# Kernel optimization log

Measured on AMD Instinct MI355X. Metric: run time of the kernel, lower is better.

Reference implementation:

```python
import jax, jax.numpy as jnp
import numpy as np

N_ACTIVE = 200000   # active voxels
GRID = 96           # spatial grid extent per axis
C = 128             # inplanes == outplanes
EPS = 1e-4          # scn BatchNormalization default eps


def _build_rulebook(n, g, seed=0):
    """Submanifold 3x3x3 rulebook: for each of 27 offsets, pairs (in_site, out_site)
    where coord[in] = coord[out] + offset and both sites are active. Padded to
    length n with dummy index n."""
    rng = np.random.default_rng(seed)
    lin = rng.choice(g ** 3, size=n, replace=False)
    coords = np.stack(np.unravel_index(lin, (g, g, g)), axis=1)  # [n,3]
    lut = -np.ones(g ** 3, dtype=np.int64)
    lut[lin] = np.arange(n)
    in_rows, out_rows = [], []
    for dx in (-1, 0, 1):
        for dy in (-1, 0, 1):
            for dz in (-1, 0, 1):
                nb = coords + np.array([dx, dy, dz])
                valid = np.all((nb >= 0) & (nb < g), axis=1)
                j = np.full(n, -1, dtype=np.int64)
                j[valid] = lut[np.ravel_multi_index(nb[valid].T, (g, g, g))]
                hit = j >= 0
                ii = j[hit]
                oi = np.nonzero(hit)[0].astype(np.int64)
                pad = n - ii.shape[0]
                in_rows.append(np.concatenate([ii, np.full(pad, n, dtype=np.int64)]))
                out_rows.append(np.concatenate([oi, np.full(pad, n, dtype=np.int64)]))
    return np.stack(in_rows), np.stack(out_rows)  # each [27, n]


def setup_inputs() -> dict:
    key = jax.random.key(0)
    k_feat, k_w1, k_w2 = jax.random.split(key, 3)
    in_idx_np, out_idx_np = _build_rulebook(N_ACTIVE, GRID)
    w_std = 1.0 / np.sqrt(27 * C)
    return {
        "features": jax.random.normal(k_feat, (N_ACTIVE, C), dtype=jnp.float32),
        "W1": jax.random.normal(k_w1, (27, C, C), dtype=jnp.float32) * w_std,
        "gamma1": jnp.ones((C,), jnp.float32),
        "beta1": jnp.zeros((C,), jnp.float32),
        "W2": jax.random.normal(k_w2, (27, C, C), dtype=jnp.float32) * w_std,
        "gamma2": jnp.ones((C,), jnp.float32),
        "beta2": jnp.zeros((C,), jnp.float32),
        "in_idx": jnp.asarray(in_idx_np),
        "out_idx": jnp.asarray(out_idx_np),
    }


def _subm_conv(feats, W, in_idx, out_idx):
    # feats: [N, Cin]; W: [27, Cin, Cout]; rulebook idx: [27, K] (dummy = N)
    n, c_in = feats.shape
    c_out = W.shape[-1]
    feats_pad = jnp.concatenate([feats, jnp.zeros((1, c_in), feats.dtype)], axis=0)

    def step(acc, t):
        ii, oi, w = t
        contrib = feats_pad[ii] @ w  # [K, Cout] gather -> GEMM
        return acc.at[oi].add(contrib), None  # scatter-add (dummy row n absorbs pad)

    acc0 = jnp.zeros((n + 1, c_out), feats.dtype)
    acc, _ = jax.lax.scan(step, acc0, (in_idx, out_idx, W))
    return acc[:n]


def _bn(x, gamma, beta):
    # batch-norm over active sites (training-mode batch stats)
    m = x.mean(axis=0)
    v = x.var(axis=0)
    return (x - m) * jax.lax.rsqrt(v + EPS) * gamma + beta


def reference(features, W1, gamma1, beta1, W2, gamma2, beta2, in_idx, out_idx):
    out = _subm_conv(features, W1, in_idx, out_idx)
    out = jax.nn.relu(_bn(out, gamma1, beta1))          # scn.BatchNormReLU
    out = _subm_conv(out, W2, in_idx, out_idx)
    out = _bn(out, gamma2, beta2)                       # scn.BatchNormalization
    return jax.nn.relu(out + features)                  # AddTable + ReLU
```

## Files before the change

### kernel.cpp

```cpp
#include <hip/hip_runtime.h>

#define NACT 200000
#define MPAD 200064
#define NBLK 1563
#define KOFF 27

#define SCAT_B 21094
#define CAST_B 25001
#define PREPW_B 1728

typedef __bf16 bf16x8 __attribute__((ext_vector_type(8)));
typedef __bf16 bf16x4 __attribute__((ext_vector_type(4)));
typedef float f32x4 __attribute__((ext_vector_type(4)));

__device__ __forceinline__ void async_load16(const void* g, void* l) {
  __builtin_amdgcn_global_load_lds(
      (__attribute__((address_space(1))) void*)g,
      (__attribute__((address_space(3))) void*)l, 16, 0, 0);
}

__global__ void prep_all(const int* __restrict__ ii, const int* __restrict__ oi,
                         int* __restrict__ G,
                         const float* __restrict__ F, __bf16* __restrict__ X,
                         const float* __restrict__ W1, const float* __restrict__ W2,
                         __bf16* __restrict__ T1, __bf16* __restrict__ T2) {
  int b = blockIdx.x;
  if (b < SCAT_B) {
    int i = b * 256 + threadIdx.x;
    if (i < KOFF * NACT) {
      int o = oi[i];
      if (o < NACT) G[(i / NACT) * MPAD + o] = ii[i];
    }
  } else if (b < SCAT_B + CAST_B) {
    int i = (b - SCAT_B) * 256 + threadIdx.x;
    if (i < (NACT + 1) * 32) {
      float4 v = (i < NACT * 32) ? ((const float4*)F)[i] : make_float4(0.f, 0.f, 0.f, 0.f);
      bf16x4 o = {(__bf16)v.x, (__bf16)v.y, (__bf16)v.z, (__bf16)v.w};
      *(bf16x4*)(X + (i << 2)) = o;
    }
  } else {
    int i = (b - SCAT_B - CAST_B) * 256 + threadIdx.x;
    int kk = i >> 14, r = i & 16383, cc = r >> 10, n = (r >> 3) & 127, e = r & 7;
    int src = (kk << 14) + ((cc << 3) + e) * 128 + n;
    T1[i] = (__bf16)W1[src];
    T2[i] = (__bf16)W2[src];
  }
}

__global__ __launch_bounds__(256, 3) void gemm_gather(
    const __bf16* __restrict__ X,
    const __bf16* __restrict__ B2,
    const int* __restrict__ G,
    __bf16* __restrict__ Y,
    float* __restrict__ Pst)
{
  __shared__ __bf16 Alds[128 * 64];
  const int t = threadIdx.x;
  const int lane = t & 63;
  const int w = t >> 6;
  const int wm = (w & 1) << 6;
  const int wn = (w >> 1) << 6;
  const int m_base = blockIdx.x << 7;
  const int r0 = t >> 3;
  const int scb = t & 7;
  const int l15 = lane & 15;
  const int q4 = lane >> 4;

  f32x4 acc[4][4];
#pragma unroll
  for (int i = 0; i < 4; ++i)
#pragma unroll
    for (int j = 0; j < 4; ++j) acc[i][j] = (f32x4){0.f, 0.f, 0.f, 0.f};

  for (int kk = 0; kk < KOFF; ++kk) {
    int rowA[4];
#pragma unroll
    for (int j = 0; j < 4; ++j) {
      int g = G[kk * MPAD + m_base + r0 + j * 32];
      rowA[j] = g < NACT ? g : NACT;
    }
#pragma unroll
    for (int s = 0; s < 2; ++s) {
      const int c0 = s << 6;
      __syncthreads();
#pragma unroll
      for (int j = 0; j < 4; ++j) {
        const int r = r0 + j * 32;
        const int gcb = scb ^ (r & 7);
        async_load16(X + (rowA[j] << 7) + c0 + (gcb << 3), &Alds[(((r << 3) + scb) << 3)]);
      }
      const __bf16* bbase = B2 + (((kk << 4) + (s << 3) + q4) << 10) + ((wn + l15) << 3);
      bf16x8 b0[4], b1[4];
#pragma unroll
      for (int ni = 0; ni < 4; ++ni)
        b0[ni] = *(const bf16x8*)(bbase + (ni << 7));
      __syncthreads();
#pragma unroll
      for (int ni = 0; ni < 4; ++ni)
        b1[ni] = *(const bf16x8*)(bbase + (1 << 12) + (ni << 7));
      {
        bf16x8 af[4];
#pragma unroll
        for (int mi = 0; mi < 4; ++mi) {
          const int r = wm + mi * 16 + l15;
          af[mi] = *(const bf16x8*)&Alds[(((r << 3) + (q4 ^ (r & 7))) << 3)];
        }
#pragma unroll
        for (int mi = 0; mi < 4; ++mi)
#pragma unroll
          for (int ni = 0; ni < 4; ++ni)
            acc[mi][ni] = __builtin_amdgcn_mfma_f32_16x16x32_bf16(
                af[mi], b0[ni], acc[mi][ni], 0, 0, 0);
      }
      {
        bf16x8 af[4];
        const int cb0 = 4 + q4;
#pragma unroll
        for (int mi = 0; mi < 4; ++mi) {
          const int r = wm + mi * 16 + l15;
          af[mi] = *(const bf16x8*)&Alds[(((r << 3) + (cb0 ^ (r & 7))) << 3)];
        }
#pragma unroll
        for (int mi = 0; mi < 4; ++mi)
#pragma unroll
          for (int ni = 0; ni < 4; ++ni)
            acc[mi][ni] = __builtin_amdgcn_mfma_f32_16x16x32_bf16(
                af[mi], b1[ni], acc[mi][ni], 0, 0, 0);
      }
    }
  }

#pragma unroll
  for (int mi = 0; mi < 4; ++mi) {
#pragma unroll
    for (int ni = 0; ni < 4; ++ni) {
      const int col = wn + ni * 16 + l15;
#pragma unroll
      for (int rg = 0; rg < 4; ++rg) {
        const int row = m_base + wm + mi * 16 + (q4 << 2) + rg;
        Y[(row << 7) + col] = (__bf16)acc[mi][ni][rg];
      }
    }
  }

  float s[4], s2[4];
#pragma unroll
  for (int ni = 0; ni < 4; ++ni) {
    float a = 0.f, b = 0.f;
#pragma unroll
    for (int mi = 0; mi < 4; ++mi)
#pragma unroll
      for (int rg = 0; rg < 4; ++rg) {
        float v = acc[mi][ni][rg];
        a += v; b += v * v;
      }
    s[ni] = a; s2[ni] = b;
  }
#pragma unroll
  for (int ni = 0; ni < 4; ++ni) {
    s[ni]  += __shfl_xor(s[ni], 16);  s[ni]  += __shfl_xor(s[ni], 32);
    s2[ni] += __shfl_xor(s2[ni], 16); s2[ni] += __shfl_xor(s2[ni], 32);
  }
  float* sc = (float*)Alds;
  __syncthreads();
  if (q4 == 0) {
#pragma unroll
    for (int ni = 0; ni < 4; ++ni) {
      sc[(w << 6) + ni * 16 + l15]       = s[ni];
      sc[256 + (w << 6) + ni * 16 + l15] = s2[ni];
    }
  }
  __syncthreads();
  {
    const int kind = t >> 7, col = t & 127;
    const int w1 = (col >> 6) << 1;
    const float v = sc[kind * 256 + (w1 << 6) + (col & 63)] +
                    sc[kind * 256 + ((w1 + 1) << 6) + (col & 63)];
    Pst[(size_t)t * NBLK + blockIdx.x] = v;
  }
}

__global__ void stats_coeffs(const float* __restrict__ P, const float* __restrict__ gamma,
                             const float* __restrict__ beta, float* __restrict__ co) {
  int c = blockIdx.x;
  float s = 0.f, s2 = 0.f;
  for (int i = threadIdx.x; i < NBLK; i += 256) {
    s  += P[(size_t)c * NBLK + i];
    s2 += P[(size_t)(128 + c) * NBLK + i];
  }
  for (int off = 32; off; off >>= 1) {
    s  += __shfl_down(s, off);
    s2 += __shfl_down(s2, off);
  }
  __shared__ float ls[8];
  if ((threadIdx.x & 63) == 0) {
    ls[threadIdx.x >> 6]     = s;
    ls[4 + (threadIdx.x >> 6)] = s2;
  }
  __syncthreads();
  if (threadIdx.x == 0) {
    float S  = ls[0] + ls[1] + ls[2] + ls[3];
    float S2 = ls[4] + ls[5] + ls[6] + ls[7];
    float m = S * (1.f / NACT);
    float v = S2 * (1.f / NACT) - m * m;
    float scale = gamma[c] * rsqrtf(v + 1e-4f);
    co[c] = scale;
    co[128 + c] = beta[c] - m * scale;
  }
}

__global__ void bn_relu_cast(const __bf16* __restrict__ Y, const float* __restrict__ co,
                             __bf16* __restrict__ X2) {
  int i = blockIdx.x * 256 + threadIdx.x;
  if (i >= (NACT + 1) * 16) return;
  bf16x8 o;
  if (i < NACT * 16) {
    bf16x8 v = ((const bf16x8*)Y)[i];
    int cg = (i & 15) << 3;
#pragma unroll
    for (int e = 0; e < 8; ++e) {
      float x = fmaf((float)v[e], co[cg + e], co[128 + cg + e]);
      o[e] = (__bf16)fmaxf(x, 0.f);
    }
  } else {
#pragma unroll
    for (int e = 0; e < 8; ++e) o[e] = (__bf16)0.f;
  }
  ((bf16x8*)X2)[i] = o;
}

__global__ void bn_add_relu(const __bf16* __restrict__ Y, const float* __restrict__ co,
                            const float* __restrict__ F, float* __restrict__ O) {
  int i = blockIdx.x * 256 + threadIdx.x;
  if (i >= NACT * 16) return;
  bf16x8 v = ((const bf16x8*)Y)[i];
  float4 f0 = ((const float4*)F)[2 * i];
  float4 f1 = ((const float4*)F)[2 * i + 1];
  int cg = (i & 15) << 3;
  float4 o0, o1;
  o0.x = fmaxf(fmaf((float)v[0], co[cg + 0], co[128 + cg + 0]) + f0.x, 0.f);
  o0.y = fmaxf(fmaf((float)v[1], co[cg + 1], co[128 + cg + 1]) + f0.y, 0.f);
  o0.z = fmaxf(fmaf((float)v[2], co[cg + 2], co[128 + cg + 2]) + f0.z, 0.f);
  o0.w = fmaxf(fmaf((float)v[3], co[cg + 3], co[128 + cg + 3]) + f0.w, 0.f);
  o1.x = fmaxf(fmaf((float)v[4], co[cg + 4], co[128 + cg + 4]) + f1.x, 0.f);
  o1.y = fmaxf(fmaf((float)v[5], co[cg + 5], co[128 + cg + 5]) + f1.y, 0.f);
  o1.z = fmaxf(fmaf((float)v[6], co[cg + 6], co[128 + cg + 6]) + f1.z, 0.f);
  o1.w = fmaxf(fmaf((float)v[7], co[cg + 7], co[128 + cg + 7]) + f1.w, 0.f);
  ((float4*)O)[2 * i] = o0;
  ((float4*)O)[2 * i + 1] = o1;
}

extern "C" void kernel_launch(void* const* d_in, const int* in_sizes, int n_in,
                              void* d_out, int out_size, void* d_ws, size_t ws_size,
                              hipStream_t stream) {
  const float* features = (const float*)d_in[0];
  const float* W1       = (const float*)d_in[1];
  const float* gamma1   = (const float*)d_in[2];
  const float* beta1    = (const float*)d_in[3];
  const float* W2       = (const float*)d_in[4];
  const float* gamma2   = (const float*)d_in[5];
  const float* beta2    = (const float*)d_in[6];
  const int* in_idx     = (const int*)d_in[7];
  const int* out_idx    = (const int*)d_in[8];

  char* ws = (char*)d_ws;
  size_t off = 0;
  int*    G   = (int*)(ws + off);    off += (size_t)KOFF * MPAD * 4;
  __bf16* X   = (__bf16*)(ws + off); off += (size_t)(NACT + 1) * 128 * 2;
  __bf16* T1  = (__bf16*)(ws + off); off += (size_t)KOFF * 128 * 128 * 2;
  __bf16* T2  = (__bf16*)(ws + off); off += (size_t)KOFF * 128 * 128 * 2;
  __bf16* Y   = (__bf16*)(ws + off); off += (size_t)MPAD * 128 * 2;
  float*  Pst = (float*)(ws + off);  off += (size_t)256 * NBLK * 4;
  float*  st  = (float*)(ws + off);  off += 4096;

  hipMemsetAsync(G, 0x7F, (size_t)KOFF * MPAD * 4, stream);

  prep_all<<<SCAT_B + CAST_B + PREPW_B, 256, 0, stream>>>(
      in_idx, out_idx, G, features, X, W1, W2, T1, T2);

  gemm_gather<<<NBLK, 256, 0, stream>>>(X, T1, G, Y, Pst);
  stats_coeffs<<<128, 256, 0, stream>>>(Pst, gamma1, beta1, st);
  bn_relu_cast<<<((NACT + 1) * 16 + 255) / 256, 256, 0, stream>>>(Y, st, X);

  gemm_gather<<<NBLK, 256, 0, stream>>>(X, T2, G, Y, Pst);
  stats_coeffs<<<128, 256, 0, stream>>>(Pst, gamma2, beta2, st + 256);
  bn_add_relu<<<(NACT * 16 + 255) / 256, 256, 0, stream>>>(Y, st + 256, features, (float*)d_out);
}
```

Before: 683.8 us.

## Enlarge gather-GEMM tile to 256x128 and stage weights through LDS

Each block now computes a 256-row by 128-column tile instead of 128x128, with each wave owning 64 rows across all 128 output columns. The weight slice is laid out as [n][c] and loaded into LDS asynchronously with the same swizzle as the gathered A rows, replacing per-lane direct global loads of pre-packed B fragments. This halves the number of blocks and per-block weight traffic per output row. The cost is more accumulator registers (launch bounds drop to 2 blocks per SM) and more shared memory, which reduces occupancy and latency hiding for the random row gathers.

```diff
diff --git a/kernel.cpp b/kernel.cpp
--- a/kernel.cpp
+++ b/kernel.cpp
@@ -1,8 +1,8 @@
 #include <hip/hip_runtime.h>
 
 #define NACT 200000
-#define MPAD 200064
-#define NBLK 1563
+#define MPAD 200192
+#define NBLK 782
 #define KOFF 27
 
 #define SCAT_B 21094
@@ -40,92 +40,87 @@
     }
   } else {
     int i = (b - SCAT_B - CAST_B) * 256 + threadIdx.x;
-    int kk = i >> 14, r = i & 16383, cc = r >> 10, n = (r >> 3) & 127, e = r & 7;
-    int src = (kk << 14) + ((cc << 3) + e) * 128 + n;
+    int k = i >> 14, r = i & 16383, n = r >> 7, c = r & 127;
+    int src = (k << 14) + (c << 7) + n;
     T1[i] = (__bf16)W1[src];
     T2[i] = (__bf16)W2[src];
   }
 }
 
-__global__ __launch_bounds__(256, 3) void gemm_gather(
+__global__ __launch_bounds__(256, 2) void gemm_gather(
     const __bf16* __restrict__ X,
-    const __bf16* __restrict__ B2,
+    const __bf16* __restrict__ WT,
     const int* __restrict__ G,
     __bf16* __restrict__ Y,
     float* __restrict__ Pst)
 {
-  __shared__ __bf16 Alds[128 * 64];
+  __shared__ __bf16 Alds[256 * 64];
+  __shared__ __bf16 Blds[128 * 64];
   const int t = threadIdx.x;
   const int lane = t & 63;
   const int w = t >> 6;
-  const int wm = (w & 1) << 6;
-  const int wn = (w >> 1) << 6;
-  const int m_base = blockIdx.x << 7;
+  const int wm = w << 6;
+  const int m_base = blockIdx.x << 8;
   const int r0 = t >> 3;
   const int scb = t & 7;
   const int l15 = lane & 15;
   const int q4 = lane >> 4;
 
-  f32x4 acc[4][4];
+  f32x4 acc[4][8];
 #pragma unroll
   for (int i = 0; i < 4; ++i)
 #pragma unroll
-    for (int j = 0; j < 4; ++j) acc[i][j] = (f32x4){0.f, 0.f, 0.f, 0.f};
+    for (int j = 0; j < 8; ++j) acc[i][j] = (f32x4){0.f, 0.f, 0.f, 0.f};
 
   for (int kk = 0; kk < KOFF; ++kk) {
-    int rowA[4];
-#pragma unroll
-    for (int j = 0; j < 4; ++j) {
+    int rowA[8];
+#pragma unroll
+    for (int j = 0; j < 8; ++j) {
       int g = G[kk * MPAD + m_base + r0 + j * 32];
       rowA[j] = g < NACT ? g : NACT;
     }
+    const __bf16* wb = WT + (kk << 14);
 #pragma unroll
     for (int s = 0; s < 2; ++s) {
       const int c0 = s << 6;
       __syncthreads();
 #pragma unroll
+      for (int j = 0; j < 8; ++j) {
+        const int r = r0 + j * 32;
+        const int gcb = scb ^ (r & 7);
+        async_load16(X + (rowA[j] << 7) + c0 + (gcb << 3), &Alds[(((r << 3) + scb) << 3)]);
+      }
+#pragma unroll
       for (int j = 0; j < 4; ++j) {
         const int r = r0 + j * 32;
         const int gcb = scb ^ (r & 7);
-        async_load16(X + (rowA[j] << 7) + c0 + (gcb << 3), &Alds[(((r << 3) + scb) << 3)]);
-      }
-      const __bf16* bbase = B2 + (((kk << 4) + (s << 3) + q4) << 10) + ((wn + l15) << 3);
-      bf16x8 b0[4], b1[4];
-#pragma unroll
-      for (int ni = 0; ni < 4; ++ni)
-        b0[ni] = *(const bf16x8*)(bbase + (ni << 7));
+        async_load16(wb + (r << 7) + c0 + (gcb << 3), &Blds[(((r << 3) + scb) << 3)]);
+      }
       __syncthreads();
 #pragma unroll
-      for (int ni = 0; ni < 4; ++ni)
-        b1[ni] = *(const bf16x8*)(bbase + (1 << 12) + (ni << 7));
-      {
+      for (int ks = 0; ks < 2; ++ks) {
+        const int cb0 = (ks << 2) + q4;
         bf16x8 af[4];
-#pragma unroll
-        for (int mi = 0; mi < 4; ++mi) {
-          const int r = wm + mi * 16 + l15;
-          af[mi] = *(const bf16x8*)&Alds[(((r << 3) + (q4 ^ (r & 7))) << 3)];
-        }
-#pragma unroll
-        for (int mi = 0; mi < 4; ++mi)
-#pragma unroll
-          for (int ni = 0; ni < 4; ++ni)
-            acc[mi][ni] = __builtin_amdgcn_mfma_f32_16x16x32_bf16(
-                af[mi], b0[ni], acc[mi][ni], 0, 0, 0);
-      }
-      {
-        bf16x8 af[4];
-        const int cb0 = 4 + q4;
 #pragma unroll
         for (int mi = 0; mi < 4; ++mi) {
           const int r = wm + mi * 16 + l15;
           af[mi] = *(const bf16x8*)&Alds[(((r << 3) + (cb0 ^ (r & 7))) << 3)];
         }
 #pragma unroll
-        for (int mi = 0; mi < 4; ++mi)
-#pragma unroll
-          for (int ni = 0; ni < 4; ++ni)
-            acc[mi][ni] = __builtin_amdgcn_mfma_f32_16x16x32_bf16(
-                af[mi], b1[ni], acc[mi][ni], 0, 0, 0);
+        for (int nh = 0; nh < 2; ++nh) {
+          bf16x8 bfr[4];
+#pragma unroll
+          for (int nn = 0; nn < 4; ++nn) {
+            const int r = (nh * 4 + nn) * 16 + l15;
+            bfr[nn] = *(const bf16x8*)&Blds[(((r << 3) + (cb0 ^ (r & 7))) << 3)];
+          }
+#pragma unroll
+          for (int mi = 0; mi < 4; ++mi)
+#pragma unroll
+            for (int nn = 0; nn < 4; ++nn)
+              acc[mi][nh * 4 + nn] = __builtin_amdgcn_mfma_f32_16x16x32_bf16(
+                  af[mi], bfr[nn], acc[mi][nh * 4 + nn], 0, 0, 0);
+        }
       }
     }
   }
@@ -133,8 +128,8 @@
 #pragma unroll
   for (int mi = 0; mi < 4; ++mi) {
 #pragma unroll
-    for (int ni = 0; ni < 4; ++ni) {
-      const int col = wn + ni * 16 + l15;
+    for (int ni = 0; ni < 8; ++ni) {
+      const int col = ni * 16 + l15;
 #pragma unroll
       for (int rg = 0; rg < 4; ++rg) {
         const int row = m_base + wm + mi * 16 + (q4 << 2) + rg;
@@ -143,9 +138,9 @@
     }
   }
 
-  float s[4], s2[4];
-#pragma unroll
-  for (int ni = 0; ni < 4; ++ni) {
+  float s[8], s2[8];
+#pragma unroll
+  for (int ni = 0; ni < 8; ++ni) {
     float a = 0.f, b = 0.f;
 #pragma unroll
     for (int mi = 0; mi < 4; ++mi)
@@ -157,7 +152,7 @@
     s[ni] = a; s2[ni] = b;
   }
 #pragma unroll
-  for (int ni = 0; ni < 4; ++ni) {
+  for (int ni = 0; ni < 8; ++ni) {
     s[ni]  += __shfl_xor(s[ni], 16);  s[ni]  += __shfl_xor(s[ni], 32);
     s2[ni] += __shfl_xor(s2[ni], 16); s2[ni] += __shfl_xor(s2[ni], 32);
   }
@@ -165,18 +160,17 @@
   __syncthreads();
   if (q4 == 0) {
 #pragma unroll
-    for (int ni = 0; ni < 4; ++ni) {
-      sc[(w << 6) + ni * 16 + l15]       = s[ni];
-      sc[256 + (w << 6) + ni * 16 + l15] = s2[ni];
+    for (int ni = 0; ni < 8; ++ni) {
+      const int col = ni * 16 + l15;
+      sc[(w << 7) + col]       = s[ni];
+      sc[512 + (w << 7) + col] = s2[ni];
     }
   }
   __syncthreads();
   {
     const int kind = t >> 7, col = t & 127;
-    const int w1 = (col >> 6) << 1;
-    const float v = sc[kind * 256 + (w1 << 6) + (col & 63)] +
-                    sc[kind * 256 + ((w1 + 1) << 6) + (col & 63)];
-    Pst[(size_t)t * NBLK + blockIdx.x] = v;
+    const float* p = sc + kind * 512 + col;
+    Pst[(size_t)t * NBLK + blockIdx.x] = p[0] + p[128] + p[256] + p[384];
   }
 }
 
@@ -194,7 +188,7 @@
   }
   __shared__ float ls[8];
   if ((threadIdx.x & 63) == 0) {
-    ls[threadIdx.x >> 6]     = s;
+    ls[threadIdx.x >> 6]       = s;
     ls[4 + (threadIdx.x >> 6)] = s2;
   }
   __syncthreads();
```

After: 614.8 us. 10.1% less time.

## Stage weight tiles in LDS, prefetch gather indices, read bf16 residual

Applied to the files above, without the earlier changes.

Weights are now stored in a plain transposed [k][n][c] layout and loaded asynchronously into a second swizzled LDS buffer alongside the gathered A tile, replacing direct per-wave global fragment loads. The next offset's gather indices are prefetched during the current offset, and the occupancy hint is raised from 3 to 4 blocks. The final residual add reads the bf16 copy of the features instead of the fp32 input, which halves that kernel's residual traffic but adds the residual at bf16 precision. A separate buffer is kept for the second-stage input so the first bf16 copy survives.

```diff
diff --git a/kernel.cpp b/kernel.cpp
--- a/kernel.cpp
+++ b/kernel.cpp
@@ -40,21 +40,22 @@
     }
   } else {
     int i = (b - SCAT_B - CAST_B) * 256 + threadIdx.x;
-    int kk = i >> 14, r = i & 16383, cc = r >> 10, n = (r >> 3) & 127, e = r & 7;
-    int src = (kk << 14) + ((cc << 3) + e) * 128 + n;
+    int k = i >> 14, r = i & 16383, n = r >> 7, c = r & 127;
+    int src = (k << 14) + (c << 7) + n;
     T1[i] = (__bf16)W1[src];
     T2[i] = (__bf16)W2[src];
   }
 }
 
-__global__ __launch_bounds__(256, 3) void gemm_gather(
+__global__ __launch_bounds__(256, 4) void gemm_gather(
     const __bf16* __restrict__ X,
-    const __bf16* __restrict__ B2,
+    const __bf16* __restrict__ WT,
     const int* __restrict__ G,
     __bf16* __restrict__ Y,
     float* __restrict__ Pst)
 {
   __shared__ __bf16 Alds[128 * 64];
+  __shared__ __bf16 Blds[128 * 64];
   const int t = threadIdx.x;
   const int lane = t & 63;
   const int w = t >> 6;
@@ -72,60 +73,57 @@
 #pragma unroll
     for (int j = 0; j < 4; ++j) acc[i][j] = (f32x4){0.f, 0.f, 0.f, 0.f};
 
+  int rowN[4];
+#pragma unroll
+  for (int j = 0; j < 4; ++j) rowN[j] = G[m_base + r0 + j * 32];
+
   for (int kk = 0; kk < KOFF; ++kk) {
     int rowA[4];
 #pragma unroll
-    for (int j = 0; j < 4; ++j) {
-      int g = G[kk * MPAD + m_base + r0 + j * 32];
-      rowA[j] = g < NACT ? g : NACT;
-    }
+    for (int j = 0; j < 4; ++j)
+      rowA[j] = (unsigned)rowN[j] < NACT ? rowN[j] : NACT;
+    const __bf16* wb = WT + (kk << 14);
 #pragma unroll
     for (int s = 0; s < 2; ++s) {
       const int c0 = s << 6;
       __syncthreads();
+#pragma unroll
+      for (int j = 0; j < 4; ++j) {
+        const int r = r0 + j * 32;
+        const int gcb = scb ^ (r & 7);
+        async_load16(wb + (r << 7) + c0 + (gcb << 3), &Blds[(((r << 3) + scb) << 3)]);
+      }
 #pragma unroll
       for (int j = 0; j < 4; ++j) {
         const int r = r0 + j * 32;
         const int gcb = scb ^ (r & 7);
         async_load16(X + (rowA[j] << 7) + c0 + (gcb << 3), &Alds[(((r << 3) + scb) << 3)]);
       }
-      const __bf16* bbase = B2 + (((kk << 4) + (s << 3) + q4) << 10) + ((wn + l15) << 3);
-      bf16x8 b0[4], b1[4];
-#pragma unroll
-      for (int ni = 0; ni < 4; ++ni)
-        b0[ni] = *(const bf16x8*)(bbase + (ni << 7));
+      if (s == 0 && kk + 1 < KOFF) {
+#pragma unroll
+        for (int j = 0; j < 4; ++j) rowN[j] = G[(kk + 1) * MPAD + m_base + r0 + j * 32];
+      }
       __syncthreads();
 #pragma unroll
-      for (int ni = 0; ni < 4; ++ni)
-        b1[ni] = *(const bf16x8*)(bbase + (1 << 12) + (ni << 7));
-      {
-        bf16x8 af[4];
-#pragma unroll
-        for (int mi = 0; mi < 4; ++mi) {
-          const int r = wm + mi * 16 + l15;
-          af[mi] = *(const bf16x8*)&Alds[(((r << 3) + (q4 ^ (r & 7))) << 3)];
-        }
-#pragma unroll
-        for (int mi = 0; mi < 4; ++mi)
-#pragma unroll
-          for (int ni = 0; ni < 4; ++ni)
-            acc[mi][ni] = __builtin_amdgcn_mfma_f32_16x16x32_bf16(
-                af[mi], b0[ni], acc[mi][ni], 0, 0, 0);
-      }
-      {
-        bf16x8 af[4];
-        const int cb0 = 4 + q4;
+      for (int ks = 0; ks < 2; ++ks) {
+        bf16x8 af[4], bfr[4];
+        const int cb0 = (ks << 2) + q4;
 #pragma unroll
         for (int mi = 0; mi < 4; ++mi) {
           const int r = wm + mi * 16 + l15;
           af[mi] = *(const bf16x8*)&Alds[(((r << 3) + (cb0 ^ (r & 7))) << 3)];
         }
 #pragma unroll
+        for (int ni = 0; ni < 4; ++ni) {
+          const int r = wn + ni * 16 + l15;
+          bfr[ni] = *(const bf16x8*)&Blds[(((r << 3) + (cb0 ^ (r & 7))) << 3)];
+        }
+#pragma unroll
         for (int mi = 0; mi < 4; ++mi)
 #pragma unroll
           for (int ni = 0; ni < 4; ++ni)
             acc[mi][ni] = __builtin_amdgcn_mfma_f32_16x16x32_bf16(
-                af[mi], b1[ni], acc[mi][ni], 0, 0, 0);
+                af[mi], bfr[ni], acc[mi][ni], 0, 0, 0);
       }
     }
   }
@@ -194,7 +192,7 @@
   }
   __shared__ float ls[8];
   if ((threadIdx.x & 63) == 0) {
-    ls[threadIdx.x >> 6]     = s;
+    ls[threadIdx.x >> 6]       = s;
     ls[4 + (threadIdx.x >> 6)] = s2;
   }
   __syncthreads();
@@ -230,22 +228,21 @@
 }
 
 __global__ void bn_add_relu(const __bf16* __restrict__ Y, const float* __restrict__ co,
-                            const float* __restrict__ F, float* __restrict__ O) {
+                            const __bf16* __restrict__ Xr, float* __restrict__ O) {
   int i = blockIdx.x * 256 + threadIdx.x;
   if (i >= NACT * 16) return;
   bf16x8 v = ((const bf16x8*)Y)[i];
-  float4 f0 = ((const float4*)F)[2 * i];
-  float4 f1 = ((const float4*)F)[2 * i + 1];
+  bf16x8 f = ((const bf16x8*)Xr)[i];
   int cg = (i & 15) << 3;
   float4 o0, o1;
-  o0.x = fmaxf(fmaf((float)v[0], co[cg + 0], co[128 + cg + 0]) + f0.x, 0.f);
-  o0.y = fmaxf(fmaf((float)v[1], co[cg + 1], co[128 + cg + 1]) + f0.y, 0.f);
-  o0.z = fmaxf(fmaf((float)v[2], co[cg + 2], co[128 + cg + 2]) + f0.z, 0.f);
-  o0.w = fmaxf(fmaf((float)v[3], co[cg + 3], co[128 + cg + 3]) + f0.w, 0.f);
-  o1.x = fmaxf(fmaf((float)v[4], co[cg + 4], co[128 + cg + 4]) + f1.x, 0.f);
-  o1.y = fmaxf(fmaf((float)v[5], co[cg + 5], co[128 + cg + 5]) + f1.y, 0.f);
-  o1.z = fmaxf(fmaf((float)v[6], co[cg + 6], co[128 + cg + 6]) + f1.z, 0.f);
-  o1.w = fmaxf(fmaf((float)v[7], co[cg + 7], co[128 + cg + 7]) + f1.w, 0.f);
+  o0.x = fmaxf(fmaf((float)v[0], co[cg + 0], co[128 + cg + 0]) + (float)f[0], 0.f);
+  o0.y = fmaxf(fmaf((float)v[1], co[cg + 1], co[128 + cg + 1]) + (float)f[1], 0.f);
+  o0.z = fmaxf(fmaf((float)v[2], co[cg + 2], co[128 + cg + 2]) + (float)f[2], 0.f);
+  o0.w = fmaxf(fmaf((float)v[3], co[cg + 3], co[128 + cg + 3]) + (float)f[3], 0.f);
+  o1.x = fmaxf(fmaf((float)v[4], co[cg + 4], co[128 + cg + 4]) + (float)f[4], 0.f);
+  o1.y = fmaxf(fmaf((float)v[5], co[cg + 5], co[128 + cg + 5]) + (float)f[5], 0.f);
+  o1.z = fmaxf(fmaf((float)v[6], co[cg + 6], co[128 + cg + 6]) + (float)f[6], 0.f);
+  o1.w = fmaxf(fmaf((float)v[7], co[cg + 7], co[128 + cg + 7]) + (float)f[7], 0.f);
   ((float4*)O)[2 * i] = o0;
   ((float4*)O)[2 * i + 1] = o1;
 }
@@ -266,7 +263,8 @@
   char* ws = (char*)d_ws;
   size_t off = 0;
   int*    G   = (int*)(ws + off);    off += (size_t)KOFF * MPAD * 4;
-  __bf16* X   = (__bf16*)(ws + off); off += (size_t)(NACT + 1) * 128 * 2;
+  __bf16* X1  = (__bf16*)(ws + off); off += (size_t)(NACT + 1) * 128 * 2;
+  __bf16* X2  = (__bf16*)(ws + off); off += (size_t)(NACT + 1) * 128 * 2;
   __bf16* T1  = (__bf16*)(ws + off); off += (size_t)KOFF * 128 * 128 * 2;
   __bf16* T2  = (__bf16*)(ws + off); off += (size_t)KOFF * 128 * 128 * 2;
   __bf16* Y   = (__bf16*)(ws + off); off += (size_t)MPAD * 128 * 2;
@@ -276,13 +274,13 @@
   hipMemsetAsync(G, 0x7F, (size_t)KOFF * MPAD * 4, stream);
 
   prep_all<<<SCAT_B + CAST_B + PREPW_B, 256, 0, stream>>>(
-      in_idx, out_idx, G, features, X, W1, W2, T1, T2);
-
-  gemm_gather<<<NBLK, 256, 0, stream>>>(X, T1, G, Y, Pst);
+      in_idx, out_idx, G, features, X1, W1, W2, T1, T2);
+
+  gemm_gather<<<NBLK, 256, 0, stream>>>(X1, T1, G, Y, Pst);
   stats_coeffs<<<128, 256, 0, stream>>>(Pst, gamma1, beta1, st);
-  bn_relu_cast<<<((NACT + 1) * 16 + 255) / 256, 256, 0, stream>>>(Y, st, X);
-
-  gemm_gather<<<NBLK, 256, 0, stream>>>(X, T2, G, Y, Pst);
+  bn_relu_cast<<<((NACT + 1) * 16 + 255) / 256, 256, 0, stream>>>(Y, st, X2);
+
+  gemm_gather<<<NBLK, 256, 0, stream>>>(X2, T2, G, Y, Pst);
   stats_coeffs<<<128, 256, 0, stream>>>(Pst, gamma2, beta2, st + 256);
-  bn_add_relu<<<(NACT * 16 + 255) / 256, 256, 0, stream>>>(Y, st + 256, features, (float*)d_out);
-}
+  bn_add_relu<<<(NACT * 16 + 255) / 256, 256, 0, stream>>>(Y, st + 256, X1, (float*)d_out);
+}
```

New measurement: 656.4 us. -4.0%, faster.
